# Optimization experiments

Measured on AMD Instinct MI355X. Metric: run time of the kernel, lower is better.

Reference implementation:

```python
import jax, jax.numpy as jnp
import numpy as np

N_NODES, N_EDGES, D_IN, D_H, N_GRAPHS = 50000, 600000, 1024, 128, 1000


def _transformer_conv(x, src, dst, wq, bq, wk, bk, wv, bv, ws, bs, n):
    """PyG TransformerConv, heads=1, concat=True, root_weight=True."""
    q = x @ wq + bq                      # [N, d]
    k = x @ wk + bk
    v = x @ wv + bv
    d = q.shape[-1]
    # per-edge attention score for edge j->i: <q_i, k_j> / sqrt(d)
    score = jnp.sum(q[dst] * k[src], axis=-1) / jnp.sqrt(jnp.asarray(d, x.dtype))  # [E]
    # segment softmax over incoming edges of each destination node
    smax = jax.ops.segment_max(score, dst, num_segments=n)
    smax = jnp.where(jnp.isfinite(smax), smax, jnp.zeros_like(smax))
    ex = jnp.exp(score - smax[dst])
    denom = jax.ops.segment_sum(ex, dst, num_segments=n)
    alpha = ex / (denom[dst] + 1e-16)
    # scatter-aggregate weighted values back to destination nodes
    agg = jax.ops.segment_sum(alpha[:, None] * v[src], dst, num_segments=n)  # [N, d]
    # skip (root) connection
    return agg + x @ ws + bs


def setup_inputs() -> dict:
    key = jax.random.key(0)
    ks = jax.random.split(key, 20)
    inp = {}
    inp['x'] = jax.random.normal(ks[0], (N_NODES, D_IN), dtype=jnp.float32)
    inp['edge_index'] = jax.random.randint(ks[1], (2, N_EDGES), 0, N_NODES, dtype=jnp.int64)
    inp['idx'] = jax.random.randint(ks[2], (N_GRAPHS,), 0, N_NODES, dtype=jnp.int64)
    s_in = 0.02
    # layer 0: 1024 -> 128
    for i, nm in enumerate(['wq0', 'wk0', 'wv0', 'ws0']):
        inp[nm] = jax.random.normal(ks[3 + i], (D_IN, D_H), dtype=jnp.float32) * s_in
    for nm in ['bq0', 'bk0', 'bv0', 'bs0']:
        inp[nm] = jnp.zeros((D_H,), dtype=jnp.float32)
    # layer 1: 128 -> 128
    for i, nm in enumerate(['wq1', 'wk1', 'wv1', 'ws1']):
        inp[nm] = jax.random.normal(ks[7 + i], (D_H, D_H), dtype=jnp.float32) * 0.08
    for nm in ['bq1', 'bk1', 'bv1', 'bs1']:
        inp[nm] = jnp.zeros((D_H,), dtype=jnp.float32)
    # MLP head 128 -> 128 -> 64 -> 1
    inp['mw1'] = jax.random.normal(ks[11], (D_H, D_H), dtype=jnp.float32) * 0.08
    inp['mb1'] = jnp.zeros((D_H,), dtype=jnp.float32)
    inp['mw2'] = jax.random.normal(ks[12], (D_H, 64), dtype=jnp.float32) * 0.08
    inp['mb2'] = jnp.zeros((64,), dtype=jnp.float32)
    inp['mw3'] = jax.random.normal(ks[13], (64, 1), dtype=jnp.float32) * 0.1
    inp['mb3'] = jnp.zeros((1,), dtype=jnp.float32)
    return inp


def reference(x, edge_index, idx,
              wq0, bq0, wk0, bk0, wv0, bv0, ws0, bs0,
              wq1, bq1, wk1, bk1, wv1, bv1, ws1, bs1,
              mw1, mb1, mw2, mb2, mw3, mb3):
    src, dst = edge_index[0], edge_index[1]
    n = x.shape[0]
    h = _transformer_conv(x, src, dst, wq0, bq0, wk0, bk0, wv0, bv0, ws0, bs0, n)
    h = jax.nn.relu(h)
    h = _transformer_conv(h, src, dst, wq1, bq1, wk1, bk1, wv1, bv1, ws1, bs1, n)
    h = jax.nn.relu(h)
    h = h[idx]                           # one center node per graph -> [B, d]
    h = jax.nn.relu(h @ mw1 + mb1)       # dropout is identity in eval
    h = jax.nn.relu(h @ mw2 + mb2)
    out = jax.nn.sigmoid(h @ mw3 + mb3)  # [B, 1]
    return out
```

## Files before the change

### kernel.cpp

```cpp
#include <hip/hip_runtime.h>
#include <hip/hip_bf16.h>
#include <cstdint>
#include <cstddef>

typedef __bf16 bf16x2 __attribute__((ext_vector_type(2)));
typedef __bf16 bf16x8 __attribute__((ext_vector_type(8)));
typedef float f32x4 __attribute__((ext_vector_type(4)));

__device__ __forceinline__ void gl_lds16(const __bf16* g, __bf16* l) {
    __builtin_amdgcn_global_load_lds(
        (const __attribute__((address_space(1))) unsigned int*)g,
        (__attribute__((address_space(3))) unsigned int*)l, 16, 0, 0);
}

template <typename AT>
__device__ __forceinline__ bf16x8 loadA8(const AT* p) {
    if constexpr (sizeof(AT) == 4) {
        float4 u = *(const float4*)p;
        float4 v = *(const float4*)(p + 4);
        return (bf16x8){(__bf16)u.x, (__bf16)u.y, (__bf16)u.z, (__bf16)u.w,
                        (__bf16)v.x, (__bf16)v.y, (__bf16)v.z, (__bf16)v.w};
    } else {
        return *(const bf16x8*)p;
    }
}

__global__ __launch_bounds__(256) void mark_idx_kernel(const int* __restrict__ idx,
                                                       int* __restrict__ flagIdx,
                                                       int* __restrict__ flagU, int B) {
    int t = blockIdx.x * 256 + threadIdx.x;
    if (t < B) {
        int n = idx[t];
        flagIdx[n] = 1;
        flagU[n] = 1;
    }
}

__global__ __launch_bounds__(256) void hist_mark_kernel(const int* __restrict__ esrc,
                                                        const int* __restrict__ edst,
                                                        const int* __restrict__ flagIdx,
                                                        int* __restrict__ deg,
                                                        int* __restrict__ flagU, int E) {
    int e = blockIdx.x * 256 + threadIdx.x;
    if (e < E) {
        int d = edst[e];
        atomicAdd(&deg[d], 1);
        if (flagIdx[d]) flagU[esrc[e]] = 1;
    }
}

__global__ __launch_bounds__(1024) void scan8_kernel(const int* __restrict__ deg,
                                                     int* __restrict__ off, int n,
                                                     const int* __restrict__ flagU,
                                                     int* __restrict__ U,
                                                     int* __restrict__ nU) {
    __shared__ int wsum[16];
    int tid = threadIdx.x, lane = tid & 63, wid = tid >> 6;
    if (tid == 0) off[0] = 0;
    int carry = 0;
    int nchunk = (n + 8191) >> 13;
    for (int c = 0; c < nchunk; ++c) {
        int base = (c << 13) + tid * 8;
        int4 a = *(const int4*)(deg + base);
        int4 b = *(const int4*)(deg + base + 4);
        int s[8];
        s[0] = a.x; s[1] = s[0] + a.y; s[2] = s[1] + a.z; s[3] = s[2] + a.w;
        s[4] = s[3] + b.x; s[5] = s[4] + b.y; s[6] = s[5] + b.z; s[7] = s[6] + b.w;
        int x = s[7];
        for (int o = 1; o < 64; o <<= 1) {
            int t = __shfl_up(x, o, 64);
            if (lane >= o) x += t;
        }
        if (lane == 63) wsum[wid] = x;
        __syncthreads();
        if (wid == 0 && lane < 16) {
            int w = wsum[lane];
            for (int o = 1; o < 16; o <<= 1) {
                int t = __shfl_up(w, o, 64);
                if (lane >= o) w += t;
            }
            wsum[lane] = w;
        }
        __syncthreads();
        int pre = carry + (wid ? wsum[wid - 1] : 0) + (x - s[7]);
#pragma unroll
        for (int i = 0; i < 8; ++i)
            if (base + i < n) off[base + i + 1] = pre + s[i];
        carry += wsum[15];
        __syncthreads();
    }
    for (int i = tid; i < n; i += 1024)
        if (flagU[i]) U[atomicAdd(nU, 1)] = i;
}

__global__ __launch_bounds__(256) void scatter_kernel(const int* __restrict__ src,
                                                      const int* __restrict__ dst,
                                                      const int* __restrict__ off,
                                                      int* __restrict__ cursor,
                                                      int* __restrict__ srcs, int E) {
    int e = blockIdx.x * 256 + threadIdx.x;
    if (e < E) {
        int d = dst[e];
        int p = off[d] + atomicAdd(&cursor[d], 1);
        srcs[p] = src[e];
    }
}

__global__ __launch_bounds__(256) void pack_w_kernel(const float* __restrict__ wq0, const float* __restrict__ wk0,
                                                     const float* __restrict__ wv0, const float* __restrict__ ws0,
                                                     const float* __restrict__ wq1, const float* __restrict__ wk1,
                                                     const float* __restrict__ wv1, const float* __restrict__ ws1,
                                                     const float* __restrict__ bq0, const float* __restrict__ bk0,
                                                     const float* __restrict__ bv0, const float* __restrict__ bs0,
                                                     const float* __restrict__ bq1, const float* __restrict__ bk1,
                                                     const float* __restrict__ bv1, const float* __restrict__ bs1,
                                                     __bf16* __restrict__ w0t, __bf16* __restrict__ w1t,
                                                     float* __restrict__ b0, float* __restrict__ b1) {
    int i = blockIdx.x * 256 + threadIdx.x;
    const int S0 = 512 * 1024, S1 = 512 * 128;
    if (i < S0) {
        int n = i >> 10, k = i & 1023;
        int sel = n >> 7, c = n & 127;
        const float* w = (sel == 0) ? wk0 : (sel == 1) ? wv0 : (sel == 2) ? wq0 : ws0;
        w0t[i] = (__bf16)w[(size_t)k * 128 + c];
    } else if (i < S0 + S1) {
        int j = i - S0;
        int n = j >> 7, k = j & 127;
        int sel = n >> 7, c = n & 127;
        const float* w = (sel == 0) ? wk1 : (sel == 1) ? wv1 : (sel == 2) ? wq1 : ws1;
        w1t[j] = (__bf16)w[(size_t)k * 128 + c];
    } else if (i < S0 + S1 + 512) {
        int t = i - S0 - S1;
        int sel = t >> 7, c = t & 127;
        const float* b = (sel == 0) ? bk0 : (sel == 1) ? bv0 : (sel == 2) ? bq0 : bs0;
        b0[t] = b[c];
    } else if (i < S0 + S1 + 1024) {
        int t = i - S0 - S1 - 512;
        int sel = t >> 7, c = t & 127;
        const float* b = (sel == 0) ? bk1 : (sel == 1) ? bv1 : (sel == 2) ? bq1 : bs1;
        b1[t] = b[c];
    }
}

template <typename AT>
__global__ __launch_bounds__(512, 4) void gemm_dual_kernel(const AT* __restrict__ A,
                                                           const __bf16* __restrict__ Bt,
                                                           const float* __restrict__ bias,
                                                           __bf16* __restrict__ outb,
                                                           float* __restrict__ outf,
                                                           const int* __restrict__ rl0,
                                                           const int* __restrict__ np0, int ns0,
                                                           const int* __restrict__ rl1,
                                                           const int* __restrict__ np1, int ns1,
                                                           int K) {
    __shared__ __align__(16) __bf16 Asl[2][128 * 32];
    __shared__ __align__(16) __bf16 Bsl[2][256 * 32];
    const int sector = blockIdx.x;
    const int* rowlist = sector ? rl1 : rl0;
    const int* nptr = sector ? np1 : np0;
    const int nrows = nptr ? *nptr : (sector ? ns1 : ns0);
    if (nrows <= 0) return;
    const __bf16* BT = Bt + (size_t)(sector ? 256 : 0) * K;
    const float* bs = bias + (sector ? 256 : 0);
    const int ntiles = (nrows + 127) >> 7;

    const int tid = threadIdx.x;
    const int lane = tid & 63, wid = tid >> 6;
    const int wm = wid >> 2, wn = wid & 3;
    const int fr = lane & 15, quad = lane >> 4;
    const int rr = tid >> 2;
    const int kc8 = (tid & 3) << 3;

    const __bf16* gB = BT + (size_t)rr * K + kc8;

    for (int mt = blockIdx.y; mt < ntiles; mt += gridDim.y) {
        const int mbase = mt << 7;
        int lr = mbase + rr;
        if (lr >= nrows) lr = nrows - 1;
        const int gr = rowlist ? rowlist[lr] : lr;
        const AT* gA = A + (size_t)gr * K + kc8;

        f32x4 acc[4][4];
#pragma unroll
        for (int i = 0; i < 4; i++)
#pragma unroll
            for (int j = 0; j < 4; j++) acc[i][j] = (f32x4){0.f, 0.f, 0.f, 0.f};

        __syncthreads();
        {
            __bf16* bd = &Bsl[0][(wid << 4) * 32];
            gl_lds16(gB, bd);
            gl_lds16(gB + (size_t)128 * K, bd + 128 * 32);
            bf16x8 a0 = loadA8(gA);
            *(bf16x8*)&Asl[0][rr * 32 + kc8] = a0;
        }
        __syncthreads();

        int cur = 0;
        for (int k0 = 0; k0 < K; k0 += 32) {
            const int kn = k0 + 32;
            const bool pf = (kn < K);
            bf16x8 aN;
            if (pf) {
                __bf16* bd = &Bsl[cur ^ 1][(wid << 4) * 32];
                gl_lds16(gB + kn, bd);
                gl_lds16(gB + (size_t)128 * K + kn, bd + 128 * 32);
                aN = loadA8(gA + kn);
            }
            bf16x8 af[4], bfr[4];
#pragma unroll
            for (int mi = 0; mi < 4; mi++)
                af[mi] = *(const bf16x8*)&Asl[cur][(wm * 64 + mi * 16 + fr) * 32 + quad * 8];
#pragma unroll
            for (int ni = 0; ni < 4; ni++)
                bfr[ni] = *(const bf16x8*)&Bsl[cur][(wn * 64 + ni * 16 + fr) * 32 + quad * 8];
#pragma unroll
            for (int mi = 0; mi < 4; mi++)
#pragma unroll
                for (int ni = 0; ni < 4; ni++)
                    acc[mi][ni] = __builtin_amdgcn_mfma_f32_16x16x32_bf16(af[mi], bfr[ni], acc[mi][ni], 0, 0, 0);
            if (pf) {
                *(bf16x8*)&Asl[cur ^ 1][rr * 32 + kc8] = aN;
                __syncthreads();
            }
            cur ^= 1;
        }

#pragma unroll
        for (int mi = 0; mi < 4; mi++)
#pragma unroll
            for (int ni = 0; ni < 4; ni++) {
                int rl = wm * 64 + mi * 16 + quad * 4;
                int cl = wn * 64 + ni * 16 + fr;
                float b = bs[cl];
#pragma unroll
                for (int r = 0; r < 4; r++) {
                    int lr2 = mbase + rl + r;
                    if (lr2 < nrows) {
                        int gr2 = rowlist ? rowlist[lr2] : lr2;
                        float v = acc[mi][ni][r] + b;
                        if (sector == 0) outb[(size_t)gr2 * 256 + cl] = (__bf16)v;
                        else             outf[(size_t)gr2 * 256 + cl] = v;
                    }
                }
            }
    }
}

__global__ __launch_bounds__(256) void attn_kernel(const float* __restrict__ qs,
                                                   const __bf16* __restrict__ kvb,
                                                   const int* __restrict__ off,
                                                   const int* __restrict__ srcs,
                                                   const int* __restrict__ nodelist,
                                                   const int* __restrict__ nptr, int nstatic,
                                                   __bf16* __restrict__ outb,
                                                   float* __restrict__ outf, int mode) {
    int n = nptr ? *nptr : nstatic;
    int lane = threadIdx.x & 63;
    int w0 = blockIdx.x * 4 + (threadIdx.x >> 6);
    int nw = gridDim.x * 4;
    const float scale = 0.08838834764831845f;
    for (int w = w0; w < n; w += nw) {
        int node = nodelist ? nodelist[w] : w;
        const float* bq = qs + (size_t)node * 256;
        float2 q = *(const float2*)(bq + 2 * lane);
        float2 s = *(const float2*)(bq + 128 + 2 * lane);
        int e0 = off[node], e1 = off[node + 1];
        float m = -INFINITY, l = 0.f;
        float ax = 0.f, ay = 0.f;
        bf16x2 kc = {(__bf16)0.f, (__bf16)0.f}, vc = kc;
        if (e0 < e1) {
            const __bf16* p = kvb + (size_t)srcs[e0] * 256;
            kc = *(const bf16x2*)(p + 2 * lane);
            vc = *(const bf16x2*)(p + 128 + 2 * lane);
        }
        for (int e = e0; e < e1; ++e) {
            bf16x2 kn = {(__bf16)0.f, (__bf16)0.f}, vn = kn;
            if (e + 1 < e1) {
                const __bf16* p = kvb + (size_t)srcs[e + 1] * 256;
                kn = *(const bf16x2*)(p + 2 * lane);
                vn = *(const bf16x2*)(p + 128 + 2 * lane);
            }
            float t = q.x * (float)kc.x + q.y * (float)kc.y;
#pragma unroll
            for (int o = 32; o > 0; o >>= 1) t += __shfl_xor(t, o, 64);
            float sc = t * scale;
            float mn = fmaxf(m, sc);
            float al = __expf(m - mn);
            float ee = __expf(sc - mn);
            ax = ax * al + ee * (float)vc.x;
            ay = ay * al + ee * (float)vc.y;
            l = l * al + ee;
            m = mn;
            kc = kn; vc = vn;
        }
        float inv = 1.f / (l + 1e-16f);
        float ox = ax * inv + s.x, oy = ay * inv + s.y;
        if (mode) {
            bf16x2 o2 = {(__bf16)fmaxf(ox, 0.f), (__bf16)fmaxf(oy, 0.f)};
            *(bf16x2*)(outb + (size_t)node * 128 + 2 * lane) = o2;
        } else {
            float2 o2 = {fmaxf(ox, 0.f), fmaxf(oy, 0.f)};
            *(float2*)(outf + (size_t)w * 128 + 2 * lane) = o2;
        }
    }
}

__global__ __launch_bounds__(128) void mlp_kernel(const float* __restrict__ hbuf,
                                                  const float* __restrict__ mw1, const float* __restrict__ mb1,
                                                  const float* __restrict__ mw2, const float* __restrict__ mb2,
                                                  const float* __restrict__ mw3, const float* __restrict__ mb3,
                                                  float* __restrict__ out, int B) {
    int b = blockIdx.x;
    int t = threadIdx.x;
    if (b >= B) return;
    __shared__ float xr[128], z1[128], z2[64];
    xr[t] = hbuf[(size_t)b * 128 + t];
    __syncthreads();
    float a1 = mb1[t];
#pragma unroll 8
    for (int k = 0; k < 128; ++k) a1 += xr[k] * mw1[k * 128 + t];
    z1[t] = fmaxf(a1, 0.f);
    __syncthreads();
    if (t < 64) {
        float a2 = mb2[t];
#pragma unroll 8
        for (int k = 0; k < 128; ++k) a2 += z1[k] * mw2[k * 64 + t];
        z2[t] = fmaxf(a2, 0.f);
    }
    __syncthreads();
    if (t < 64) {
        float p = z2[t] * mw3[t];
#pragma unroll
        for (int o = 32; o > 0; o >>= 1) p += __shfl_xor(p, o, 64);
        if (t == 0) out[b] = 1.f / (1.f + __expf(-(p + mb3[0])));
    }
}

extern "C" void kernel_launch(void* const* d_in, const int* in_sizes, int n_in,
                              void* d_out, int out_size, void* d_ws, size_t ws_size,
                              hipStream_t stream) {
    const float* x   = (const float*)d_in[0];
    const int*   ei  = (const int*)d_in[1];
    const int*   idx = (const int*)d_in[2];
    const float* wq0 = (const float*)d_in[3];
    const float* wk0 = (const float*)d_in[4];
    const float* wv0 = (const float*)d_in[5];
    const float* ws0 = (const float*)d_in[6];
    const float* bq0 = (const float*)d_in[7];
    const float* bk0 = (const float*)d_in[8];
    const float* bv0 = (const float*)d_in[9];
    const float* bs0 = (const float*)d_in[10];
    const float* wq1 = (const float*)d_in[11];
    const float* wk1 = (const float*)d_in[12];
    const float* wv1 = (const float*)d_in[13];
    const float* ws1 = (const float*)d_in[14];
    const float* bq1 = (const float*)d_in[15];
    const float* bk1 = (const float*)d_in[16];
    const float* bv1 = (const float*)d_in[17];
    const float* bs1 = (const float*)d_in[18];
    const float* mw1 = (const float*)d_in[19];
    const float* mb1 = (const float*)d_in[20];
    const float* mw2 = (const float*)d_in[21];
    const float* mb2 = (const float*)d_in[22];
    const float* mw3 = (const float*)d_in[23];
    const float* mb3 = (const float*)d_in[24];
    float* out = (float*)d_out;

    const int Nn = in_sizes[0] / 1024;
    const int E  = in_sizes[1] / 2;
    const int B  = in_sizes[2];
    const int* esrc = ei;
    const int* edst = ei + E;
    const int degPad = ((Nn + 8191) >> 13) << 13;

    uintptr_t base = (uintptr_t)d_ws;
    auto alloc = [&](size_t bytes) -> void* {
        uintptr_t p = (base + 255) & ~(uintptr_t)255;
        base = p + bytes;
        return (void*)p;
    };
    __bf16* kvb  = (__bf16*)alloc((size_t)Nn * 256 * 2);
    __bf16* kv1b = kvb;
    float*  qs   = (float*)alloc((size_t)Nn * 256 * 4);
    float*  qs1  = qs;
    __bf16* h0b  = (__bf16*)alloc((size_t)Nn * 128 * 2);
    float*  hbuf = (float*)alloc((size_t)B * 128 * 4);
    __bf16* w0t  = (__bf16*)alloc(512 * 1024 * 2);
    __bf16* w1t  = (__bf16*)alloc(512 * 128 * 2);
    float*  b0   = (float*)alloc(512 * 4);
    float*  b1   = (float*)alloc(512 * 4);
    int* deg     = (int*)alloc((size_t)degPad * 4);
    int* cursor  = (int*)alloc((size_t)Nn * 4);
    int* flagIdx = (int*)alloc((size_t)Nn * 4);
    int* flagU   = (int*)alloc((size_t)Nn * 4);
    int* nU      = (int*)alloc(256);
    size_t zbytes = (uintptr_t)nU + 256 - (uintptr_t)deg;
    int* off     = (int*)alloc((size_t)(Nn + 1) * 4);
    int* srcs    = (int*)alloc((size_t)E * 4);
    int* U       = (int*)alloc((size_t)Nn * 4);

    hipMemsetAsync(deg, 0, zbytes, stream);

    mark_idx_kernel<<<(B + 255) / 256, 256, 0, stream>>>(idx, flagIdx, flagU, B);
    hist_mark_kernel<<<(E + 255) / 256, 256, 0, stream>>>(esrc, edst, flagIdx, deg, flagU, E);
    scan8_kernel<<<1, 1024, 0, stream>>>(deg, off, Nn, flagU, U, nU);
    scatter_kernel<<<(E + 255) / 256, 256, 0, stream>>>(esrc, edst, off, cursor, srcs, E);

    pack_w_kernel<<<(512 * 1024 + 512 * 128 + 1024 + 255) / 256, 256, 0, stream>>>(
        wq0, wk0, wv0, ws0, wq1, wk1, wv1, ws1,
        bq0, bk0, bv0, bs0, bq1, bk1, bv1, bs1, w0t, w1t, b0, b1);

    const int mtiles = (Nn + 127) / 128;

    gemm_dual_kernel<float><<<dim3(2, mtiles), 512, 0, stream>>>(x, w0t, b0, kvb, qs,
                                                                 nullptr, nullptr, Nn,
                                                                 U, nU, 0, 1024);
    attn_kernel<<<4096, 256, 0, stream>>>(qs, kvb, off, srcs, U, nU, 0, h0b, nullptr, 1);

    gemm_dual_kernel<__bf16><<<dim3(2, 128), 512, 0, stream>>>(h0b, w1t, b1, kv1b, qs1,
                                                               U, nU, 0,
                                                               idx, nullptr, B, 128);
    attn_kernel<<<(B + 3) / 4, 256, 0, stream>>>(qs1, kv1b, off, srcs, idx, nullptr, B, nullptr, hbuf, 0);

    mlp_kernel<<<B, 128, 0, stream>>>(hbuf, mw1, mb1, mw2, mb2, mw3, mb3, out, B);
}
```

Baseline: 651.4 us.

## Triple-buffer B tiles, prefetch two steps ahead, and rebalance GEMM grid sectors

The dual GEMM now keeps three LDS buffers for the weight tile and issues async global-to-LDS loads two k-steps ahead. Raw A values are held in registers and converted to bf16 one step later, so load latency is hidden behind MFMA work. The full __syncthreads is replaced by an lgkmcnt wait plus s_barrier. The 2D grid becomes a 1D grid with an uneven split between sectors, giving the smaller second sector (U rows or idx rows) fewer blocks instead of an equal count. The extra B buffer raises LDS use per block, which may limit occupancy under the 4-blocks launch bound.

Result: faster. 572.1 us (-12.2%).

```diff
diff --git a/kernel.cpp b/kernel.cpp
--- a/kernel.cpp
+++ b/kernel.cpp
@@ -13,15 +13,27 @@
         (__attribute__((address_space(3))) unsigned int*)l, 16, 0, 0);
 }
 
+template <typename AT> struct ARaw;
+template <> struct ARaw<float>  { float4 u, v; };
+template <> struct ARaw<__bf16> { bf16x8 w; };
+
 template <typename AT>
-__device__ __forceinline__ bf16x8 loadA8(const AT* p) {
+__device__ __forceinline__ void loadAraw(const AT* p, ARaw<AT>& r) {
     if constexpr (sizeof(AT) == 4) {
-        float4 u = *(const float4*)p;
-        float4 v = *(const float4*)(p + 4);
-        return (bf16x8){(__bf16)u.x, (__bf16)u.y, (__bf16)u.z, (__bf16)u.w,
-                        (__bf16)v.x, (__bf16)v.y, (__bf16)v.z, (__bf16)v.w};
+        r.u = *(const float4*)p;
+        r.v = *(const float4*)(p + 4);
     } else {
-        return *(const bf16x8*)p;
+        r.w = *(const bf16x8*)p;
+    }
+}
+
+template <typename AT>
+__device__ __forceinline__ bf16x8 cvtA(const ARaw<AT>& r) {
+    if constexpr (sizeof(AT) == 4) {
+        return (bf16x8){(__bf16)r.u.x, (__bf16)r.u.y, (__bf16)r.u.z, (__bf16)r.u.w,
+                        (__bf16)r.v.x, (__bf16)r.v.y, (__bf16)r.v.z, (__bf16)r.v.w};
+    } else {
+        return r.w;
     }
 }
 
@@ -152,10 +164,13 @@
                                                            const int* __restrict__ np0, int ns0,
                                                            const int* __restrict__ rl1,
                                                            const int* __restrict__ np1, int ns1,
-                                                           int K) {
+                                                           int K, int s0blocks) {
     __shared__ __align__(16) __bf16 Asl[2][128 * 32];
-    __shared__ __align__(16) __bf16 Bsl[2][256 * 32];
-    const int sector = blockIdx.x;
+    __shared__ __align__(16) __bf16 Bsl[3][256 * 32];
+    const int bx = blockIdx.x;
+    const int sector = (bx >= s0blocks) ? 1 : 0;
+    const int tile0  = sector ? bx - s0blocks : bx;
+    const int tstr   = sector ? (gridDim.x - s0blocks) : s0blocks;
     const int* rowlist = sector ? rl1 : rl0;
     const int* nptr = sector ? np1 : np0;
     const int nrows = nptr ? *nptr : (sector ? ns1 : ns0);
@@ -163,6 +178,7 @@
     const __bf16* BT = Bt + (size_t)(sector ? 256 : 0) * K;
     const float* bs = bias + (sector ? 256 : 0);
     const int ntiles = (nrows + 127) >> 7;
+    const int NT = K >> 5;
 
     const int tid = threadIdx.x;
     const int lane = tid & 63, wid = tid >> 6;
@@ -172,8 +188,9 @@
     const int kc8 = (tid & 3) << 3;
 
     const __bf16* gB = BT + (size_t)rr * K + kc8;
-
-    for (int mt = blockIdx.y; mt < ntiles; mt += gridDim.y) {
+    __bf16* const bdB = (__bf16*)0 + ((size_t)(wid << 4) * 32);
+
+    for (int mt = tile0; mt < ntiles; mt += tstr) {
         const int mbase = mt << 7;
         int lr = mbase + rr;
         if (lr >= nrows) lr = nrows - 1;
@@ -187,43 +204,54 @@
             for (int j = 0; j < 4; j++) acc[i][j] = (f32x4){0.f, 0.f, 0.f, 0.f};
 
         __syncthreads();
+
+        ARaw<AT> a0, aC;
         {
-            __bf16* bd = &Bsl[0][(wid << 4) * 32];
-            gl_lds16(gB, bd);
-            gl_lds16(gB + (size_t)128 * K, bd + 128 * 32);
-            bf16x8 a0 = loadA8(gA);
-            *(bf16x8*)&Asl[0][rr * 32 + kc8] = a0;
-        }
-        __syncthreads();
-
-        int cur = 0;
-        for (int k0 = 0; k0 < K; k0 += 32) {
-            const int kn = k0 + 32;
-            const bool pf = (kn < K);
-            bf16x8 aN;
+            __bf16* bd0 = &Bsl[0][(size_t)(wid << 4) * 32];
+            gl_lds16(gB, bd0);
+            gl_lds16(gB + (size_t)128 * K, bd0 + 128 * 32);
+            loadAraw(gA, a0);
+            __bf16* bd1 = &Bsl[1][(size_t)(wid << 4) * 32];
+            gl_lds16(gB + 32, bd1);
+            gl_lds16(gB + (size_t)128 * K + 32, bd1 + 128 * 32);
+            loadAraw(gA + 32, aC);
+            *(bf16x8*)&Asl[0][rr * 32 + kc8] = cvtA<AT>(a0);
+            asm volatile("s_waitcnt lgkmcnt(0)" ::: "memory");
+            __builtin_amdgcn_s_barrier();
+        }
+
+        for (int k = 0; k < NT; ++k) {
+            const __bf16* As = Asl[k & 1];
+            const __bf16* Bs = Bsl[k % 3];
+            bf16x8 af[4];
+#pragma unroll
+            for (int mi = 0; mi < 4; mi++)
+                af[mi] = *(const bf16x8*)&As[(wm * 64 + mi * 16 + fr) * 32 + quad * 8];
+#pragma unroll
+            for (int ni = 0; ni < 4; ni++) {
+                bf16x8 b8 = *(const bf16x8*)&Bs[(wn * 64 + ni * 16 + fr) * 32 + quad * 8];
+#pragma unroll
+                for (int mi = 0; mi < 4; mi++)
+                    acc[mi][ni] = __builtin_amdgcn_mfma_f32_16x16x32_bf16(af[mi], b8, acc[mi][ni], 0, 0, 0);
+            }
+            const bool wr = (k + 1 < NT);
+            const bool pf = (k + 2 < NT);
             if (pf) {
-                __bf16* bd = &Bsl[cur ^ 1][(wid << 4) * 32];
+                const int kn = (k + 2) << 5;
+                __bf16* bd = &Bsl[(k + 2) % 3][(size_t)(wid << 4) * 32];
                 gl_lds16(gB + kn, bd);
                 gl_lds16(gB + (size_t)128 * K + kn, bd + 128 * 32);
-                aN = loadA8(gA + kn);
-            }
-            bf16x8 af[4], bfr[4];
-#pragma unroll
-            for (int mi = 0; mi < 4; mi++)
-                af[mi] = *(const bf16x8*)&Asl[cur][(wm * 64 + mi * 16 + fr) * 32 + quad * 8];
-#pragma unroll
-            for (int ni = 0; ni < 4; ni++)
-                bfr[ni] = *(const bf16x8*)&Bsl[cur][(wn * 64 + ni * 16 + fr) * 32 + quad * 8];
-#pragma unroll
-            for (int mi = 0; mi < 4; mi++)
-#pragma unroll
-                for (int ni = 0; ni < 4; ni++)
-                    acc[mi][ni] = __builtin_amdgcn_mfma_f32_16x16x32_bf16(af[mi], bfr[ni], acc[mi][ni], 0, 0, 0);
+            }
+            if (wr) {
+                *(bf16x8*)&Asl[(k + 1) & 1][rr * 32 + kc8] = cvtA<AT>(aC);
+            }
             if (pf) {
-                *(bf16x8*)&Asl[cur ^ 1][rr * 32 + kc8] = aN;
-                __syncthreads();
-            }
-            cur ^= 1;
+                loadAraw(gA + ((k + 2) << 5), aC);
+            }
+            if (wr) {
+                asm volatile("s_waitcnt lgkmcnt(0)" ::: "memory");
+                __builtin_amdgcn_s_barrier();
+            }
         }
 
 #pragma unroll
@@ -413,14 +441,14 @@
 
     const int mtiles = (Nn + 127) / 128;
 
-    gemm_dual_kernel<float><<<dim3(2, mtiles), 512, 0, stream>>>(x, w0t, b0, kvb, qs,
-                                                                 nullptr, nullptr, Nn,
-                                                                 U, nU, 0, 1024);
+    gemm_dual_kernel<float><<<mtiles + 121, 512, 0, stream>>>(x, w0t, b0, kvb, qs,
+                                                              nullptr, nullptr, Nn,
+                                                              U, nU, 0, 1024, mtiles);
     attn_kernel<<<4096, 256, 0, stream>>>(qs, kvb, off, srcs, U, nU, 0, h0b, nullptr, 1);
 
-    gemm_dual_kernel<__bf16><<<dim3(2, 128), 512, 0, stream>>>(h0b, w1t, b1, kv1b, qs1,
-                                                               U, nU, 0,
-                                                               idx, nullptr, B, 128);
+    gemm_dual_kernel<__bf16><<<144, 512, 0, stream>>>(h0b, w1t, b1, kv1b, qs1,
+                                                      U, nU, 0,
+                                                      idx, nullptr, B, 128, 128);
     attn_kernel<<<(B + 3) / 4, 256, 0, stream>>>(qs1, kv1b, off, srcs, idx, nullptr, B, nullptr, hbuf, 0);
 
     mlp_kernel<<<B, 128, 0, stream>>>(hbuf, mw1, mb1, mw2, mb2, mw3, mb3, out, B);
```
